# Performance work log

Measured on AMD Instinct MI355X. Metric: run time of the kernel, lower is better.

Reference implementation:

```python
import jax, jax.numpy as jnp
import numpy as np

B, S, H = 4, 2048, 512
DEPTH, EXP = 2, 4
MAX_LR = 0.1
C = 8            # n_chunks
L = S // C       # chunk length
HE = H * EXP


def _l2norm(x, eps=1e-12):
    n = jnp.sqrt(jnp.sum(x * x, axis=-1, keepdims=True))
    return x / jnp.maximum(n, eps)


def _mem_fwd(mw1, mb1, mw2, mb2, x):
    # ResLinear: residual MLP blocks, x <- x + W2 @ silu(W1 @ x + b1) + b2
    for d in range(DEPTH):
        h = jax.nn.silu(x @ mw1[d].T + mb1[d])
        x = x + h @ mw2[d].T + mb2[d]
    return x


def setup_inputs() -> dict:
    key = jax.random.key(0)
    ks = jax.random.split(key, 9)
    s = 1.0 / np.sqrt(H)
    s2 = 1.0 / np.sqrt(HE)
    return {
        "x": jax.random.normal(ks[0], (B, S, H), jnp.float32),
        "wq": jax.random.normal(ks[1], (H, H), jnp.float32) * s, "bq": jnp.zeros((H,), jnp.float32),
        "wk": jax.random.normal(ks[2], (H, H), jnp.float32) * s, "bk": jnp.zeros((H,), jnp.float32),
        "wv": jax.random.normal(ks[3], (H, H), jnp.float32) * s, "bv": jnp.zeros((H,), jnp.float32),
        "wlr": jax.random.normal(ks[4], (1, H), jnp.float32) * s, "blr": jnp.zeros((1,), jnp.float32),
        "wf": jax.random.normal(ks[5], (1, H), jnp.float32) * s, "bf": jnp.zeros((1,), jnp.float32),
        "wm": jax.random.normal(ks[6], (1, H), jnp.float32) * s, "bm": jnp.zeros((1,), jnp.float32),
        "mw1": jax.random.normal(ks[7], (DEPTH, HE, H), jnp.float32) * s,
        "mb1": jnp.zeros((DEPTH, HE), jnp.float32),
        "mw2": jax.random.normal(ks[8], (DEPTH, H, HE), jnp.float32) * s2,
        "mb2": jnp.zeros((DEPTH, H), jnp.float32),
        "mom_w1": jnp.zeros((DEPTH, HE, H), jnp.float32),
        "mom_b1": jnp.zeros((DEPTH, HE), jnp.float32),
        "mom_w2": jnp.zeros((DEPTH, H, HE), jnp.float32),
        "mom_b2": jnp.zeros((DEPTH, H), jnp.float32),
    }


def reference(x, wq, bq, wk, bk, wv, bv, wlr, blr, wf, bf, wm, bm,
              mw1, mb1, mw2, mb2, mom_w1, mom_b1, mom_w2, mom_b2):
    # projections (non-generating path; S % C == 0 so no padding)
    q = _l2norm(x @ wq.T + bq)                            # [B,S,H]
    k = _l2norm(x @ wk.T + bk).reshape(B, C, L, H)
    v = (x @ wv.T + bv).reshape(B, C, L, H)
    lr = jax.nn.sigmoid(x @ wlr.T + blr).reshape(B, C, L, 1) * MAX_LR
    forget = jax.nn.sigmoid(x @ wf.T + bf).reshape(B, C, L, 1)
    momg = jax.nn.sigmoid(x @ wm.T + bm).reshape(B, C, L, 1)

    mem = (mw1, mb1, mw2, mb2)

    def chunk_loss(mem_params, k_c, v_c, lr_c):
        # k_c,v_c: [B,L,H]; lr_c: [B,L,1]
        preds = _mem_fwd(*mem_params, k_c)
        loss = jnp.mean((preds - v_c) ** 2, axis=-1)      # [B,L]
        return jnp.sum(loss * lr_c[..., 0])

    # per-chunk synthetic gradients of the memory MLP, then mean over chunks
    grads = jax.vmap(jax.grad(chunk_loss), in_axes=(None, 1, 1, 1))(mem, k, v, lr)
    grads = jax.tree_util.tree_map(lambda g: jnp.mean(g, axis=0), grads)

    alpha = jnp.mean(forget, axis=(1, 2, 3))              # [B] forget gate
    theta = jnp.mean(lr, axis=(1, 2, 3))                  # [B] adaptive lr
    eta = jnp.mean(momg, axis=(1, 2, 3))                  # [B] momentum gate

    def update(p, g, m):
        shp = (B,) + (1,) * p.ndim
        a, t, e = alpha.reshape(shp), theta.reshape(shp), eta.reshape(shp)
        m_b = e * m[None] - t * g[None]                   # [B,*p.shape]
        return jnp.mean(p[None] * (1.0 - a) + m_b, axis=0)

    moms = (mom_w1, mom_b1, mom_w2, mom_b2)
    new_mem = tuple(update(p, g, m) for p, g, m in zip(mem, grads, moms))

    return _mem_fwd(*new_mem, q)                          # [B,S,H]
```

## Files before the change

### kernel.cpp

```cpp
#include <hip/hip_runtime.h>
#include <cstdint>
#include <cstddef>


#define NROWS 8192
#define HDIM  512
#define HEDIM 2048
#define NCHUNK 8
#define BK    64
#define DPCOEF (2.0f / (HDIM * NCHUNK))

typedef unsigned short u16;
typedef __attribute__((ext_vector_type(8))) unsigned short u16x8;
typedef __attribute__((ext_vector_type(8))) short bf16x8;
typedef __attribute__((ext_vector_type(4))) float f32x4;

__device__ __forceinline__ float sigmoidf_(float x){ return 1.0f/(1.0f+__expf(-x)); }
__device__ __forceinline__ float siluf_(float x){ return x*sigmoidf_(x); }
__device__ __forceinline__ float dsiluf_(float x){ float s=sigmoidf_(x); return s*(1.0f+x*(1.0f-s)); }
__device__ __forceinline__ u16 bf1_(float x){
    union{float f; unsigned u;} v; v.f = x;
    return (u16)((v.u + 0x7fffu + ((v.u>>16)&1u)) >> 16);
}
__device__ __forceinline__ unsigned bfpack_(float a, float b){
    union{float f; unsigned u;} ua, ub; ua.f = a; ub.f = b;
    unsigned ra = (ua.u + 0x7fffu + ((ua.u>>16)&1u)) >> 16;
    unsigned rb = (ub.u + 0x7fffu + ((ub.u>>16)&1u)) & 0xffff0000u;
    return ra | rb;
}
__device__ __forceinline__ float bf2f_(u16 h){
    union{unsigned u; float f;} v; v.u = ((unsigned)h) << 16; return v.f;
}
__device__ __forceinline__ int swkey_(int row){
    return (((row>>3)&1)<<2) | (((row>>4)&1)<<1) | ((row>>5)&1);
}
__device__ __forceinline__ void gl_lds16(const u16* g, u16* l){
    __builtin_amdgcn_global_load_lds(
        (const __attribute__((address_space(1))) unsigned*)g,
        (__attribute__((address_space(3))) unsigned*)l, 16, 0, 0);
}
__device__ __forceinline__ void bar_(){ asm volatile("s_barrier" ::: "memory"); }
#define VMCNT8  asm volatile("s_waitcnt vmcnt(8)" ::: "memory")
#define VMCNT0  asm volatile("s_waitcnt vmcnt(0)" ::: "memory")
#define LGKM0   asm volatile("s_waitcnt lgkmcnt(0)" ::: "memory")

template<int MODE, bool ATR, bool CSUM>
__global__ __launch_bounds__(256)
void mgemm_k(const u16* __restrict__ A, const u16* __restrict__ B,
             const float* __restrict__ bias, const float* __restrict__ resF,
             const u16* __restrict__ resB, const u16* __restrict__ aux,
             const float* __restrict__ lrs,
             float* __restrict__ outF, u16* __restrict__ outB, u16* __restrict__ outB2,
             float* __restrict__ cpart,
             int M, int N, int K, int lda, int ldb, int ldv)
{
    constexpr int NBUF = ATR ? 1 : 2;
    __shared__ __align__(128) u16 As[NBUF][128*64];
    __shared__ __align__(128) u16 Bs[NBUF][128*64];
    const int tid = threadIdx.x;
    const int lane = tid & 63, wvi = tid >> 6;
    const int wm = wvi >> 1, wn = wvi & 1;
    const int lr = lane & 15, lq = lane >> 4;

    const int gx = gridDim.x;
    const int nwg = gx * gridDim.y;
    int bid = blockIdx.y * gx + blockIdx.x;
    bid = (bid & 7) * (nwg >> 3) + (bid >> 3);
    const int m0 = (bid / gx) * 128, n0 = (bid % gx) * 128;

    int kbeg = 0, kend = K;
    if (MODE == 3){ const int ks = K >> 4; kbeg = blockIdx.z * ks; kend = kbeg + ks; }
    const int nk = (kend - kbeg) / BK;

    f32x4 acc[4][4];
    const f32x4 zz = {0.f,0.f,0.f,0.f};
    #pragma unroll
    for (int i = 0; i < 4; ++i)
        #pragma unroll
        for (int j = 0; j < 4; ++j) acc[i][j] = zz;

    const int mc = tid & 15, kp = tid >> 4;
    const int tkey = (((mc&1)<<2)|(((mc>>1)&1)<<1)|((mc>>2)&1));
    const int tcs = ((kp >> 1) ^ tkey) * 8 + (kp & 1) * 4;
    u16x8 rgA0, rgA1, rgA2, rgA3, rgB0, rgB1, rgB2, rgB3;

    auto stageNT = [&](int k0, int b){
        #pragma unroll
        for (int it = 0; it < 4; ++it){
            const int seg = it*4 + wvi;
            const int key = (((seg&1)<<2)|(((seg>>1)&1)<<1)|((seg>>2)&1));
            const int row = seg*8 + (lane>>3);
            const int chunk = (lane&7) ^ key;
            gl_lds16(A + (size_t)(m0+row)*lda + k0 + chunk*8, &As[b][seg*512]);
            gl_lds16(B + (size_t)(n0+row)*ldb + k0 + chunk*8, &Bs[b][seg*512]);
        }
    };
    auto gloadTN = [&](int k0){
        const u16* pa = A + (size_t)(k0 + 4*kp) * lda + m0 + mc*8;
        rgA0 = *(const u16x8*)pa;          rgA1 = *(const u16x8*)(pa + lda);
        rgA2 = *(const u16x8*)(pa+2*lda);  rgA3 = *(const u16x8*)(pa + 3*lda);
        const u16* pb = B + (size_t)(k0 + 4*kp) * ldb + n0 + mc*8;
        rgB0 = *(const u16x8*)pb;          rgB1 = *(const u16x8*)(pb + ldb);
        rgB2 = *(const u16x8*)(pb+2*ldb);  rgB3 = *(const u16x8*)(pb + 3*ldb);
    };
    auto dswriteTN = [&](){
        #pragma unroll
        for (int j = 0; j < 8; ++j){
            uint2 w;
            w.x = (unsigned)rgA0[j] | ((unsigned)rgA1[j] << 16);
            w.y = (unsigned)rgA2[j] | ((unsigned)rgA3[j] << 16);
            *(uint2*)&As[0][(mc*8 + j)*64 + tcs] = w;
            uint2 v;
            v.x = (unsigned)rgB0[j] | ((unsigned)rgB1[j] << 16);
            v.y = (unsigned)rgB2[j] | ((unsigned)rgB3[j] << 16);
            *(uint2*)&Bs[0][(mc*8 + j)*64 + tcs] = v;
        }
    };
    auto mfmaStep = [&](int b){
        #pragma unroll
        for (int ks = 0; ks < 2; ++ks) {
            bf16x8 afr[4], bfr[4];
            #pragma unroll
            for (int i = 0; i < 4; ++i){
                const int ra = wm*64 + i*16 + lr, rb = wn*64 + i*16 + lr;
                afr[i] = *(const bf16x8*)&As[b][ra*64 + (((ks*4 + lq) ^ swkey_(ra)) << 3)];
                bfr[i] = *(const bf16x8*)&Bs[b][rb*64 + (((ks*4 + lq) ^ swkey_(rb)) << 3)];
            }
            #pragma unroll
            for (int mi = 0; mi < 4; ++mi)
                #pragma unroll
                for (int ni = 0; ni < 4; ++ni)
                    acc[mi][ni] = __builtin_amdgcn_mfma_f32_16x16x32_bf16(afr[mi], bfr[ni], acc[mi][ni], 0, 0, 0);
        }
    };

    if (!ATR) {
        stageNT(kbeg, 0);
        int cur = 0;
        for (int i = 0; i < nk; ++i){
            const int k0 = kbeg + i*BK;
            if (i + 1 < nk){ stageNT(k0 + BK, cur ^ 1); VMCNT8; }
            else           { VMCNT0; }
            bar_();
            mfmaStep(cur);
            bar_();
            cur ^= 1;
        }
    } else {
        gloadTN(kbeg);
        dswriteTN();
        LGKM0;
        __syncthreads();
        for (int i = 0; i < nk; ++i){
            const int k0 = kbeg + i*BK;
            const bool hn = (i + 1 < nk);
            if (hn) gloadTN(k0 + BK);
            mfmaStep(0);
            __syncthreads();
            if (hn){ dswriteTN(); LGKM0; }
            __syncthreads();
        }
    }

    if (MODE == 3){
        unsigned* P32 = (unsigned*)outB;
        const size_t zb = (size_t)blockIdx.z * ((size_t)M * N / 2);
        #pragma unroll
        for (int ni = 0; ni < 4; ++ni){
            const int col = n0 + wn*64 + ni*16 + lr;
            #pragma unroll
            for (int mi = 0; mi < 4; ++mi){
                const int pr = (m0 + wm*64 + mi*16 + lq*4) >> 1;
                P32[zb + (size_t)pr*N + col]     = bfpack_(acc[mi][ni][0], acc[mi][ni][1]);
                P32[zb + (size_t)(pr+1)*N + col] = bfpack_(acc[mi][ni][2], acc[mi][ni][3]);
            }
        }
        return;
    }

    if (MODE == 7){
        #pragma unroll
        for (int ni = 0; ni < 4; ++ni){
            const int col = n0 + wn*64 + ni*16 + lr;
            const float bv = bias[col];
            #pragma unroll
            for (int mi = 0; mi < 4; ++mi){
                const int rbase = m0 + wm*64 + mi*16 + lq*4;
                #pragma unroll
                for (int v = 0; v < 4; ++v){
                    const size_t idx = (size_t)(rbase + v) * N + col;
                    outF[idx] = acc[mi][ni][v] + bv + resF[idx];
                }
            }
        }
        return;
    }

    u16*  S   = (u16*)&As[0][0];
    u16*  S2  = (u16*)&Bs[0][0];
    float* red = (float*)&Bs[0][0];
    float cs[4] = {0.f, 0.f, 0.f, 0.f};
    __syncthreads();
    #pragma unroll
    for (int ni = 0; ni < 4; ++ni){
        const int cl = wn*64 + ni*16 + lr;
        const int col = n0 + cl;
        float bv = 0.0f;
        if (MODE==1 || MODE==2 || MODE==6 || MODE==8 || MODE==9 || MODE==10) bv = bias[col];
        #pragma unroll
        for (int mi = 0; mi < 4; ++mi){
            #pragma unroll
            for (int v = 0; v < 4; ++v){
                const int rl = wm*64 + mi*16 + lq*4 + v;
                const int row = m0 + rl;
                const size_t idx = (size_t)row * N + col;
                const float o = acc[mi][ni][v];
                const int sidx = rl*128 + (cl ^ (((rl>>2)&3)<<4));
                float t;
                if (MODE == 1){
                    const float u = o + bv;
                    t = siluf_(u);
                    S2[sidx] = bf1_(dsiluf_(u));
                }
                else if (MODE == 2){ t = siluf_(o + bv); }
                else if (MODE == 4){ t = o * bf2f_(aux[idx]); if (CSUM) cs[ni] += t; }
                else if (MODE == 5){ t = o + bf2f_(resB[idx]); if (CSUM) cs[ni] += t; }
                else if (MODE == 6){ t = o + bv + resF[idx]; outF[idx] = t; }
                else if (MODE == 8){
                    const float u = o + bv + bf2f_(resB[idx]);
                    t = lrs[row] * DPCOEF * (u - bf2f_(aux[(size_t)row * ldv + col]));
                    if (CSUM) cs[ni] += t;
                }
                else if (MODE == 9){ t = o + bv + bf2f_(resB[idx]); }
                else { t = o + bv; }
                S[sidx] = bf1_(t);
            }
        }
    }
    if (CSUM){
        #pragma unroll
        for (int ni = 0; ni < 4; ++ni)
            red[(wm*4 + lq)*128 + wn*64 + ni*16 + lr] = cs[ni];
    }
    __syncthreads();
    #pragma unroll
    for (int j = 0; j < 8; ++j){
        const int ix = j*256 + tid;
        const int rl = ix >> 4, cc = (ix & 15) << 3;
        *(u16x8*)(outB + (size_t)(m0 + rl) * N + n0 + cc)
            = *(const u16x8*)&S[rl*128 + (cc ^ (((rl>>2)&3)<<4))];
    }
    if (MODE == 1){
        #pragma unroll
        for (int j = 0; j < 8; ++j){
            const int ix = j*256 + tid;
            const int rl = ix >> 4, cc = (ix & 15) << 3;
            *(u16x8*)(outB2 + (size_t)(m0 + rl) * N + n0 + cc)
                = *(const u16x8*)&S2[rl*128 + (cc ^ (((rl>>2)&3)<<4))];
        }
    }
    if (CSUM && tid < 128){
        float s = 0.f;
        #pragma unroll
        for (int z = 0; z < 8; ++z) s += red[z*128 + tid];
        cpart[(size_t)(m0 >> 7) * N + n0 + tid] = s;
    }
}

#define XSLOTS   (NROWS*HDIM/8)
#define W1S      (2*HEDIM*HDIM/8)
#define KVQSLOTS (3*HDIM*HDIM/8)
#define NB_EW    ((XSLOTS + 2*W1S + KVQSLOTS)/256 + 7)
#define TTILE    1024
__global__ __launch_bounds__(256)
void prep_all_k(const float* __restrict__ x,  u16* __restrict__ xb,
                const float* __restrict__ mw1, u16* __restrict__ mw1b,
                const float* __restrict__ mw2, u16* __restrict__ mw2b,
                const float* __restrict__ wk, const float* __restrict__ wv,
                const float* __restrict__ wq, u16* __restrict__ wkvqb,
                const float* __restrict__ bk, const float* __restrict__ bv,
                const float* __restrict__ bq, float* __restrict__ bkvq,
                u16* __restrict__ mw2Tb, u16* __restrict__ mw1T1b)
{
    __shared__ float tile[32][33];
    const int blk = blockIdx.x;
    if (blk >= NB_EW){
        int tj = blk - NB_EW;
        const float* in; u16* outp; int R, C;
        if (tj < TTILE){
            in = mw2; outp = mw2Tb; R = HDIM; C = HEDIM;
        } else if (tj < 2*TTILE){
            in = mw2 + (size_t)HDIM*HEDIM; outp = mw2Tb + (size_t)HEDIM*HDIM;
            R = HDIM; C = HEDIM; tj -= TTILE;
        } else {
            in = mw1 + (size_t)HEDIM*HDIM; outp = mw1T1b;
            R = HEDIM; C = HDIM; tj -= 2*TTILE;
        }
        const int tpc = C/32;
        const int r0 = (tj / tpc) * 32, c0 = (tj % tpc) * 32;
        const int tx = threadIdx.x & 31, ty = threadIdx.x >> 5;
        #pragma unroll
        for (int j = 0; j < 4; ++j)
            tile[ty + 8*j][tx] = in[(size_t)(r0 + ty + 8*j) * C + c0 + tx];
        __syncthreads();
        #pragma unroll
        for (int j = 0; j < 4; ++j)
            outp[(size_t)(c0 + ty + 8*j) * R + r0 + tx] = bf1_(tile[tx][ty + 8*j]);
        return;
    }
    const int id = blk * 256 + threadIdx.x;
    const float* src; u16* dst; int i;
    if (id < XSLOTS){ src = x; dst = xb; i = id; }
    else if (id < XSLOTS + W1S){ src = mw1; dst = mw1b; i = id - XSLOTS; }
    else if (id < XSLOTS + 2*W1S){ src = mw2; dst = mw2b; i = id - XSLOTS - W1S; }
    else if (id < XSLOTS + 2*W1S + KVQSLOTS){
        const int j = id - XSLOTS - 2*W1S;
        const int per = HDIM*HDIM/8;
        src = (j < per) ? wk : (j < 2*per ? wv : wq);
        i = (j < per) ? j : (j < 2*per ? j - per : j - 2*per);
        dst = wkvqb + ((size_t)(j - i)) * 8;
    }
    else {
        const int j = id - XSLOTS - 2*W1S - KVQSLOTS;
        if (j < 3*HDIM)
            bkvq[j] = (j < HDIM) ? bk[j] : (j < 2*HDIM ? bv[j-HDIM] : bq[j-2*HDIM]);
        return;
    }
    const float4 a = *(const float4*)(src + (size_t)i*8);
    const float4 b = *(const float4*)(src + (size_t)i*8 + 4);
    u16x8 o;
    o[0]=bf1_(a.x); o[1]=bf1_(a.y); o[2]=bf1_(a.z); o[3]=bf1_(a.w);
    o[4]=bf1_(b.x); o[5]=bf1_(b.y); o[6]=bf1_(b.z); o[7]=bf1_(b.w);
    *(u16x8*)(dst + (size_t)i*8) = o;
}

template<bool WF32>
__global__ __launch_bounds__(64)
void l2norm_k(const u16* __restrict__ in, int ld,
              float* __restrict__ outF, u16* __restrict__ outB)
{
    const u16* p = in + (size_t)blockIdx.x * ld;
    const int t = threadIdx.x;
    u16x8 v = *(const u16x8*)(p + t*8);
    float f[8];
    #pragma unroll
    for (int j = 0; j < 8; ++j) f[j] = bf2f_(v[j]);
    float s = 0.f;
    #pragma unroll
    for (int j = 0; j < 8; ++j) s += f[j]*f[j];
    #pragma unroll
    for (int o = 1; o < 64; o <<= 1) s += __shfl_xor(s, o);
    const float sc = 1.0f / fmaxf(sqrtf(s), 1e-12f);
    #pragma unroll
    for (int j = 0; j < 8; ++j) f[j] *= sc;
    if (WF32){
        float* q = outF + (size_t)blockIdx.x * HDIM + t*8;
        *(float4*)q     = make_float4(f[0], f[1], f[2], f[3]);
        *(float4*)(q+4) = make_float4(f[4], f[5], f[6], f[7]);
    }
    u16x8 ob;
    #pragma unroll
    for (int j = 0; j < 8; ++j) ob[j] = bf1_(f[j]);
    *(u16x8*)(outB + (size_t)blockIdx.x * HDIM + t*8) = ob;
}

__global__ __launch_bounds__(64)
void gates_k(const float* __restrict__ x,
             const float* __restrict__ wlr, const float* __restrict__ blr,
             const float* __restrict__ wf,  const float* __restrict__ bfp,
             const float* __restrict__ wm,  const float* __restrict__ bm,
             float* __restrict__ lr_s, float* __restrict__ f_s, float* __restrict__ m_s)
{
    const size_t row = blockIdx.x;
    const float* p = x + row * HDIM;
    const int t = threadIdx.x;
    float s0 = 0.f, s1 = 0.f, s2 = 0.f;
    #pragma unroll
    for (int i = 0; i < 8; i += 4){
        float4 xv = *(const float4*)(p   + t*8 + i);
        float4 a  = *(const float4*)(wlr + t*8 + i);
        float4 b  = *(const float4*)(wf  + t*8 + i);
        float4 c  = *(const float4*)(wm  + t*8 + i);
        s0 += xv.x*a.x + xv.y*a.y + xv.z*a.z + xv.w*a.w;
        s1 += xv.x*b.x + xv.y*b.y + xv.z*b.z + xv.w*b.w;
        s2 += xv.x*c.x + xv.y*c.y + xv.z*c.z + xv.w*c.w;
    }
    #pragma unroll
    for (int o = 1; o < 64; o <<= 1){
        s0 += __shfl_xor(s0, o); s1 += __shfl_xor(s1, o); s2 += __shfl_xor(s2, o);
    }
    if (t == 0){
        lr_s[row] = sigmoidf_(s0 + blr[0]) * 0.1f;
        f_s[row]  = sigmoidf_(s1 + bfp[0]);
        m_s[row]  = sigmoidf_(s2 + bm[0]);
    }
}

__global__ __launch_bounds__(256)
void scalars_k(const float* __restrict__ lr_s, const float* __restrict__ f_s,
               const float* __restrict__ m_s, float* __restrict__ sc)
{
    __shared__ float sh0[256], sh1[256], sh2[256];
    const int t = threadIdx.x;
    float s0 = 0.f, s1 = 0.f, s2 = 0.f;
    for (int i = t; i < NROWS; i += 256){ s0 += f_s[i]; s1 += lr_s[i]; s2 += m_s[i]; }
    sh0[t] = s0; sh1[t] = s1; sh2[t] = s2;
    __syncthreads();
    for (int o = 128; o > 0; o >>= 1){
        if (t < o){ sh0[t] += sh0[t+o]; sh1[t] += sh1[t+o]; sh2[t] += sh2[t+o]; }
        __syncthreads();
    }
    if (t == 0){
        sc[0] = sh0[0] / (float)NROWS;
        sc[1] = sh1[0] / (float)NROWS;
        sc[2] = sh2[0] / (float)NROWS;
    }
}

__global__ __launch_bounds__(256)
void colsum_upd_k(const float* __restrict__ part, const float* __restrict__ p,
                  const float* __restrict__ mom, const float* __restrict__ sc,
                  float* __restrict__ nb, int cols)
{
    const int c = blockIdx.x * 256 + threadIdx.x;
    if (c < cols){
        float s = 0.f;
        for (int r = 0; r < 64; ++r) s += part[(size_t)r * cols + c];
        nb[c] = p[c] * (1.0f - sc[0]) + sc[2] * mom[c] - sc[1] * s;
    }
}

__global__ __launch_bounds__(256)
void fupdate16p_k(const float* __restrict__ p, const unsigned* __restrict__ P32,
                  const float* __restrict__ mom, const float* __restrict__ sc,
                  u16* __restrict__ nWb, int N, int MN2)
{
    const int i = blockIdx.x * 256 + threadIdx.x;
    if (i < MN2){
        float g0 = 0.f, g1 = 0.f;
        #pragma unroll
        for (int z = 0; z < 16; ++z){
            const unsigned w = P32[(size_t)z * MN2 + i];
            g0 += bf2f_((u16)(w & 0xffffu));
            g1 += bf2f_((u16)(w >> 16));
        }
        const int c = i & (N - 1);
        const size_t r0 = ((size_t)(i / N) * 2) * N + c;
        nWb[r0]     = bf1_(p[r0]     * (1.0f - sc[0]) + sc[2] * mom[r0]     - sc[1] * g0);
        nWb[r0 + N] = bf1_(p[r0 + N] * (1.0f - sc[0]) + sc[2] * mom[r0 + N] - sc[1] * g1);
    }
}

extern "C" void kernel_launch(void* const* d_in, const int* in_sizes, int n_in,
                              void* d_out, int out_size, void* d_ws, size_t ws_size,
                              hipStream_t stream)
{
    const float* x      = (const float*)d_in[0];
    const float* wq     = (const float*)d_in[1];
    const float* bq     = (const float*)d_in[2];
    const float* wk     = (const float*)d_in[3];
    const float* bk     = (const float*)d_in[4];
    const float* wv     = (const float*)d_in[5];
    const float* bv     = (const float*)d_in[6];
    const float* wlr    = (const float*)d_in[7];
    const float* blr    = (const float*)d_in[8];
    const float* wf     = (const float*)d_in[9];
    const float* bfp    = (const float*)d_in[10];
    const float* wm     = (const float*)d_in[11];
    const float* bm     = (const float*)d_in[12];
    const float* mw1    = (const float*)d_in[13];
    const float* mb1    = (const float*)d_in[14];
    const float* mw2    = (const float*)d_in[15];
    const float* mb2    = (const float*)d_in[16];
    const float* mom_w1 = (const float*)d_in[17];
    const float* mom_b1 = (const float*)d_in[18];
    const float* mom_w2 = (const float*)d_in[19];
    const float* mom_b2 = (const float*)d_in[20];
    float* out = (float*)d_out;

    char* base = (char*)d_ws;
    size_t off = 0;
    auto alloc = [&](size_t bytes)->char*{ char* p = base + off; off += (bytes + 255) & ~(size_t)255; return p; };
    const size_t NHf  = (size_t)NROWS * HDIM  * 4;
    const size_t NHb  = (size_t)NROWS * HDIM  * 2;
    const size_t NHEb = (size_t)NROWS * HEDIM * 2;
    const int    WHALF = HEDIM * HDIM;

    float* F2   = (float*)alloc(NHf);
    u16*  xb    = (u16*) alloc(NHb);
    u16*  kb    = (u16*) alloc(NHb);
    u16*  x1b   = (u16*) alloc(NHb);
    u16*  g2b   = (u16*) alloc(NHb);
    u16*  hb    = (u16*) alloc(NHEb);
    u16*  db    = (u16*) alloc(NHEb);
    u16*  dhb   = (u16*) alloc(NHEb + NHf);
    u16*  wkvqb = (u16*) alloc((size_t)3*HDIM*HDIM*2);
    float* bkvq = (float*)alloc((size_t)3*HDIM*4);
    u16*  mw1b  = (u16*) alloc((size_t)2*WHALF*2);
    u16*  mw2b  = (u16*) alloc((size_t)2*WHALF*2);
    u16*  mw2Tb = (u16*) alloc((size_t)2*WHALF*2);
    u16*  mw1T1b= (u16*) alloc((size_t)WHALF*2);
    u16*  nW1b  = (u16*) alloc((size_t)2*WHALF*2);
    u16*  nW2b  = (u16*) alloc((size_t)2*WHALF*2);
    float* cpart= (float*)alloc((size_t)64*HEDIM*4);
    float* lr_s = (float*)alloc((size_t)NROWS*4);
    float* f_s  = (float*)alloc((size_t)NROWS*4);
    float* m_s  = (float*)alloc((size_t)NROWS*4);
    float* sc   = (float*)alloc(64);
    float* nb1  = (float*)alloc((size_t)2*HEDIM*4);
    float* nb2  = (float*)alloc((size_t)2*HDIM*4);

    u16* qb  = xb;
    u16* g1b = g2b;
    u16* P3b = dhb;
    float* F1 = (float*)((char*)dhb + NHEb);
    unsigned* Pp = (unsigned*)db;

    const dim3 blk(256);
    const dim3 gKVQ (3*HDIM/128, NROWS/128);
    const dim3 gN512 (HDIM/128,  NROWS/128);
    const dim3 gN2048(HEDIM/128, NROWS/128);
    const dim3 gTN2  (HEDIM/128, HDIM/128, 16);
    const dim3 gTN1  (HDIM/128,  HEDIM/128, 16);
    const int MN2 = WHALF / 2;

    const float* mw1_1 = mw1 + (size_t)WHALF;
    const float* mw2_1 = mw2 + (size_t)WHALF;

    #define GARG(Ab,Bb,bi,rF,rB,ax,ll,oF,oB,oB2,cp,M,N,K,la,lb,lv) \
        ((const u16*)(Ab),(const u16*)(Bb),(const float*)(bi),(const float*)(rF),\
         (const u16*)(rB),(const u16*)(ax),(const float*)(ll),\
         (float*)(oF),(u16*)(oB),(u16*)(oB2),(float*)(cp),(M),(N),(K),(la),(lb),(lv))

    prep_all_k<<<dim3(NB_EW + 3*TTILE), blk, 0, stream>>>(
        x, xb, mw1, mw1b, mw2, mw2b, wk, wv, wq, wkvqb,
        bk, bv, bq, bkvq, mw2Tb, mw1T1b);
    gates_k<<<NROWS, 64, 0, stream>>>(x, wlr, blr, wf, bfp, wm, bm, lr_s, f_s, m_s);
    scalars_k<<<1, blk, 0, stream>>>(lr_s, f_s, m_s, sc);

    mgemm_k<10,false,false><<<gKVQ, blk, 0, stream>>>GARG(xb, wkvqb, bkvq, 0,0,0,0, 0, P3b, 0, 0, NROWS,3*HDIM,HDIM, HDIM,HDIM, 0);
    l2norm_k<false><<<NROWS, 64, 0, stream>>>(P3b,          3*HDIM, nullptr, kb);
    l2norm_k<true ><<<NROWS, 64, 0, stream>>>(P3b + 2*HDIM, 3*HDIM, F2, qb);

    mgemm_k<2,false,false><<<gN2048, blk, 0, stream>>>GARG(kb, mw1b, mb1, 0,0,0,0, 0, hb, 0, 0, NROWS,HEDIM,HDIM, HDIM,HDIM, 0);
    mgemm_k<9,false,false><<<gN512, blk, 0, stream>>>GARG(hb, mw2b, mb2, 0, kb, 0,0, 0, x1b, 0, 0, NROWS,HDIM,HEDIM, HEDIM,HEDIM, 0);
    mgemm_k<1,false,false><<<gN2048, blk, 0, stream>>>GARG(x1b, mw1b+WHALF, mb1+HEDIM, 0,0,0,0, 0, hb, db, 0, NROWS,HEDIM,HDIM, HDIM,HDIM, 0);
    mgemm_k<8,false,true><<<gN512, blk, 0, stream>>>GARG(hb, mw2b+WHALF, mb2+HDIM, 0, x1b, P3b + HDIM, lr_s, 0, g2b, 0, cpart, NROWS,HDIM,HEDIM, HEDIM,HEDIM, 3*HDIM);

    colsum_upd_k<<<dim3(HDIM/256), blk, 0, stream>>>(cpart, mb2+HDIM, mom_b2+HDIM, sc, nb2+HDIM, HDIM);
    mgemm_k<4,false,true><<<gN2048, blk, 0, stream>>>GARG(g2b, mw2Tb+WHALF, 0,0,0, db, 0, 0, dhb, 0, cpart, NROWS,HEDIM,HDIM, HDIM,HDIM, 0);
    mgemm_k<3,true,false><<<gTN2, blk, 0, stream>>>GARG(g2b, hb, 0,0,0,0,0, 0, Pp, 0, 0, HDIM,HEDIM,NROWS, HDIM,HEDIM, 0);
    fupdate16p_k<<<dim3((MN2+255)/256), blk, 0, stream>>>(mw2_1, Pp, mom_w2+WHALF, sc, nW2b+WHALF, HEDIM, MN2);
    colsum_upd_k<<<dim3(HEDIM/256), blk, 0, stream>>>(cpart, mb1+HEDIM, mom_b1+HEDIM, sc, nb1+HEDIM, HEDIM);
    mgemm_k<3,true,false><<<gTN1, blk, 0, stream>>>GARG(dhb, x1b, 0,0,0,0,0, 0, Pp, 0, 0, HEDIM,HDIM,NROWS, HEDIM,HDIM, 0);
    fupdate16p_k<<<dim3((MN2+255)/256), blk, 0, stream>>>(mw1_1, Pp, mom_w1+WHALF, sc, nW1b+WHALF, HDIM, MN2);
    mgemm_k<5,false,true><<<gN512, blk, 0, stream>>>GARG(dhb, mw1T1b, 0, 0, g2b, 0, 0, 0, g1b, 0, cpart, NROWS,HDIM,HEDIM, HEDIM,HEDIM, 0);

    colsum_upd_k<<<dim3(HDIM/256), blk, 0, stream>>>(cpart, mb2, mom_b2, sc, nb2, HDIM);
    mgemm_k<1,false,false><<<gN2048, blk, 0, stream>>>GARG(kb, mw1b, mb1, 0,0,0,0, 0, hb, db, 0, NROWS,HEDIM,HDIM, HDIM,HDIM, 0);
    mgemm_k<4,false,true><<<gN2048, blk, 0, stream>>>GARG(g1b, mw2Tb, 0,0,0, db, 0, 0, dhb, 0, cpart, NROWS,HEDIM,HDIM, HDIM,HDIM, 0);
    mgemm_k<3,true,false><<<gTN2, blk, 0, stream>>>GARG(g1b, hb, 0,0,0,0,0, 0, Pp, 0, 0, HDIM,HEDIM,NROWS, HDIM,HEDIM, 0);
    fupdate16p_k<<<dim3((MN2+255)/256), blk, 0, stream>>>(mw2, Pp, mom_w2, sc, nW2b, HEDIM, MN2);
    colsum_upd_k<<<dim3(HEDIM/256), blk, 0, stream>>>(cpart, mb1, mom_b1, sc, nb1, HEDIM);
    mgemm_k<3,true,false><<<gTN1, blk, 0, stream>>>GARG(dhb, kb, 0,0,0,0,0, 0, Pp, 0, 0, HEDIM,HDIM,NROWS, HEDIM,HDIM, 0);
    fupdate16p_k<<<dim3((MN2+255)/256), blk, 0, stream>>>(mw1, Pp, mom_w1, sc, nW1b, HDIM, MN2);

    mgemm_k<2,false,false><<<gN2048, blk, 0, stream>>>GARG(qb, nW1b, nb1, 0,0,0,0, 0, hb, 0, 0, NROWS,HEDIM,HDIM, HDIM,HDIM, 0);
    mgemm_k<6,false,false><<<gN512, blk, 0, stream>>>GARG(hb, nW2b, nb2, F2, 0,0,0, F1, x1b, 0, 0, NROWS,HDIM,HEDIM, HEDIM,HEDIM, 0);
    mgemm_k<2,false,false><<<gN2048, blk, 0, stream>>>GARG(x1b, nW1b+WHALF, nb1+HEDIM, 0,0,0,0, 0, hb, 0, 0, NROWS,HEDIM,HDIM, HDIM,HDIM, 0);
    mgemm_k<7,false,false><<<gN512, blk, 0, stream>>>GARG(hb, nW2b+WHALF, nb2+HDIM, F1, 0,0,0, out, 0, 0, 0, NROWS,HDIM,HEDIM, HEDIM,HEDIM, 0);

    #undef GARG
    (void)in_sizes; (void)n_in; (void)out_size; (void)ws_size;
}
```

Before: 687.7 us.

## Use 64x128 two-wave tiles for the N=512 GEMMs to fill more CUs

Adds a WAVES template parameter to the GEMM kernel. For the long-K GEMMs with N=512, the M tile shrinks from 128 to 64 rows and the block drops from four waves to two, which doubles the number of workgroups. The staging loops, vmcnt waits, epilogue indexing and column-sum partial counts are adjusted to match, and colsum_upd_k now takes the partial count as a parameter. The aim is to give the skinny-N GEMMs enough workgroups to occupy all CUs, at the cost of less B-tile reuse per block and more column-sum partials to reduce.

```diff
diff --git a/kernel.cpp b/kernel.cpp
--- a/kernel.cpp
+++ b/kernel.cpp
@@ -40,12 +40,13 @@
         (__attribute__((address_space(3))) unsigned*)l, 16, 0, 0);
 }
 __device__ __forceinline__ void bar_(){ asm volatile("s_barrier" ::: "memory"); }
+#define VMCNT12 asm volatile("s_waitcnt vmcnt(12)" ::: "memory")
 #define VMCNT8  asm volatile("s_waitcnt vmcnt(8)" ::: "memory")
 #define VMCNT0  asm volatile("s_waitcnt vmcnt(0)" ::: "memory")
 #define LGKM0   asm volatile("s_waitcnt lgkmcnt(0)" ::: "memory")
 
-template<int MODE, bool ATR, bool CSUM>
-__global__ __launch_bounds__(256)
+template<int MODE, bool ATR, bool CSUM, int WAVES>
+__global__ __launch_bounds__(WAVES*64)
 void mgemm_k(const u16* __restrict__ A, const u16* __restrict__ B,
              const float* __restrict__ bias, const float* __restrict__ resF,
              const u16* __restrict__ resB, const u16* __restrict__ aux,
@@ -55,18 +56,22 @@
              int M, int N, int K, int lda, int ldb, int ldv)
 {
     constexpr int NBUF = ATR ? 1 : 2;
-    __shared__ __align__(128) u16 As[NBUF][128*64];
+    constexpr int MT   = (WAVES == 4) ? 128 : 64;
+    constexpr int NT_  = WAVES * 64;
+    __shared__ __align__(128) u16 As[NBUF][MT*64];
     __shared__ __align__(128) u16 Bs[NBUF][128*64];
     const int tid = threadIdx.x;
     const int lane = tid & 63, wvi = tid >> 6;
-    const int wm = wvi >> 1, wn = wvi & 1;
+    const int wm = (WAVES == 4) ? (wvi >> 1) : 0;
+    const int wn = (WAVES == 4) ? (wvi & 1) : wvi;
+    constexpr int WNW = (WAVES == 4) ? 2 : 2;
     const int lr = lane & 15, lq = lane >> 4;
 
     const int gx = gridDim.x;
     const int nwg = gx * gridDim.y;
     int bid = blockIdx.y * gx + blockIdx.x;
     bid = (bid & 7) * (nwg >> 3) + (bid >> 3);
-    const int m0 = (bid / gx) * 128, n0 = (bid % gx) * 128;
+    const int m0 = (bid / gx) * MT, n0 = (bid % gx) * 128;
 
     int kbeg = 0, kend = K;
     if (MODE == 3){ const int ks = K >> 4; kbeg = blockIdx.z * ks; kend = kbeg + ks; }
@@ -86,12 +91,19 @@
 
     auto stageNT = [&](int k0, int b){
         #pragma unroll
-        for (int it = 0; it < 4; ++it){
-            const int seg = it*4 + wvi;
+        for (int it = 0; it < (MT/8)/WAVES; ++it){
+            const int seg = it*WAVES + wvi;
             const int key = (((seg&1)<<2)|(((seg>>1)&1)<<1)|((seg>>2)&1));
             const int row = seg*8 + (lane>>3);
             const int chunk = (lane&7) ^ key;
             gl_lds16(A + (size_t)(m0+row)*lda + k0 + chunk*8, &As[b][seg*512]);
+        }
+        #pragma unroll
+        for (int it = 0; it < 16/WAVES; ++it){
+            const int seg = it*WAVES + wvi;
+            const int key = (((seg&1)<<2)|(((seg>>1)&1)<<1)|((seg>>2)&1));
+            const int row = seg*8 + (lane>>3);
+            const int chunk = (lane&7) ^ key;
             gl_lds16(B + (size_t)(n0+row)*ldb + k0 + chunk*8, &Bs[b][seg*512]);
         }
     };
@@ -139,8 +151,10 @@
         int cur = 0;
         for (int i = 0; i < nk; ++i){
             const int k0 = kbeg + i*BK;
-            if (i + 1 < nk){ stageNT(k0 + BK, cur ^ 1); VMCNT8; }
-            else           { VMCNT0; }
+            if (i + 1 < nk){
+                stageNT(k0 + BK, cur ^ 1);
+                if (WAVES == 4) { VMCNT8; } else { VMCNT12; }
+            } else { VMCNT0; }
             bar_();
             mfmaStep(cur);
             bar_();
@@ -199,6 +213,7 @@
     u16*  S   = (u16*)&As[0][0];
     u16*  S2  = (u16*)&Bs[0][0];
     float* red = (float*)&Bs[0][0];
+    constexpr int RED = (WAVES == 4) ? 8 : 4;
     float cs[4] = {0.f, 0.f, 0.f, 0.f};
     __syncthreads();
     #pragma unroll
@@ -245,7 +260,7 @@
     __syncthreads();
     #pragma unroll
     for (int j = 0; j < 8; ++j){
-        const int ix = j*256 + tid;
+        const int ix = j*NT_ + tid;
         const int rl = ix >> 4, cc = (ix & 15) << 3;
         *(u16x8*)(outB + (size_t)(m0 + rl) * N + n0 + cc)
             = *(const u16x8*)&S[rl*128 + (cc ^ (((rl>>2)&3)<<4))];
@@ -253,7 +268,7 @@
     if (MODE == 1){
         #pragma unroll
         for (int j = 0; j < 8; ++j){
-            const int ix = j*256 + tid;
+            const int ix = j*NT_ + tid;
             const int rl = ix >> 4, cc = (ix & 15) << 3;
             *(u16x8*)(outB2 + (size_t)(m0 + rl) * N + n0 + cc)
                 = *(const u16x8*)&S2[rl*128 + (cc ^ (((rl>>2)&3)<<4))];
@@ -262,8 +277,8 @@
     if (CSUM && tid < 128){
         float s = 0.f;
         #pragma unroll
-        for (int z = 0; z < 8; ++z) s += red[z*128 + tid];
-        cpart[(size_t)(m0 >> 7) * N + n0 + tid] = s;
+        for (int z = 0; z < RED; ++z) s += red[z*128 + tid];
+        cpart[(size_t)(m0 / MT) * N + n0 + tid] = s;
     }
 }
 
@@ -420,12 +435,12 @@
 __global__ __launch_bounds__(256)
 void colsum_upd_k(const float* __restrict__ part, const float* __restrict__ p,
                   const float* __restrict__ mom, const float* __restrict__ sc,
-                  float* __restrict__ nb, int cols)
+                  float* __restrict__ nb, int cols, int nparts)
 {
     const int c = blockIdx.x * 256 + threadIdx.x;
     if (c < cols){
         float s = 0.f;
-        for (int r = 0; r < 64; ++r) s += part[(size_t)r * cols + c];
+        for (int r = 0; r < nparts; ++r) s += part[(size_t)r * cols + c];
         nb[c] = p[c] * (1.0f - sc[0]) + sc[2] * mom[c] - sc[1] * s;
     }
 }
@@ -516,10 +531,10 @@
     float* F1 = (float*)((char*)dhb + NHEb);
     unsigned* Pp = (unsigned*)db;
 
-    const dim3 blk(256);
-    const dim3 gKVQ (3*HDIM/128, NROWS/128);
-    const dim3 gN512 (HDIM/128,  NROWS/128);
-    const dim3 gN2048(HEDIM/128, NROWS/128);
+    const dim3 blk(256), blk2(128);
+    const dim3 gKVQ  (3*HDIM/128, NROWS/128);
+    const dim3 gN512 (HDIM/128,   NROWS/64);
+    const dim3 gN2048(HEDIM/128,  NROWS/128);
     const dim3 gTN2  (HEDIM/128, HDIM/128, 16);
     const dim3 gTN1  (HDIM/128,  HEDIM/128, 16);
     const int MN2 = WHALF / 2;
@@ -538,37 +553,37 @@
     gates_k<<<NROWS, 64, 0, stream>>>(x, wlr, blr, wf, bfp, wm, bm, lr_s, f_s, m_s);
     scalars_k<<<1, blk, 0, stream>>>(lr_s, f_s, m_s, sc);
 
-    mgemm_k<10,false,false><<<gKVQ, blk, 0, stream>>>GARG(xb, wkvqb, bkvq, 0,0,0,0, 0, P3b, 0, 0, NROWS,3*HDIM,HDIM, HDIM,HDIM, 0);
+    mgemm_k<10,false,false,4><<<gKVQ, blk, 0, stream>>>GARG(xb, wkvqb, bkvq, 0,0,0,0, 0, P3b, 0, 0, NROWS,3*HDIM,HDIM, HDIM,HDIM, 0);
     l2norm_k<false><<<NROWS, 64, 0, stream>>>(P3b,          3*HDIM, nullptr, kb);
     l2norm_k<true ><<<NROWS, 64, 0, stream>>>(P3b + 2*HDIM, 3*HDIM, F2, qb);
 
-    mgemm_k<2,false,false><<<gN2048, blk, 0, stream>>>GARG(kb, mw1b, mb1, 0,0,0,0, 0, hb, 0, 0, NROWS,HEDIM,HDIM, HDIM,HDIM, 0);
-    mgemm_k<9,false,false><<<gN512, blk, 0, stream>>>GARG(hb, mw2b, mb2, 0, kb, 0,0, 0, x1b, 0, 0, NROWS,HDIM,HEDIM, HEDIM,HEDIM, 0);
-    mgemm_k<1,false,false><<<gN2048, blk, 0, stream>>>GARG(x1b, mw1b+WHALF, mb1+HEDIM, 0,0,0,0, 0, hb, db, 0, NROWS,HEDIM,HDIM, HDIM,HDIM, 0);
-    mgemm_k<8,false,true><<<gN512, blk, 0, stream>>>GARG(hb, mw2b+WHALF, mb2+HDIM, 0, x1b, P3b + HDIM, lr_s, 0, g2b, 0, cpart, NROWS,HDIM,HEDIM, HEDIM,HEDIM, 3*HDIM);
-
-    colsum_upd_k<<<dim3(HDIM/256), blk, 0, stream>>>(cpart, mb2+HDIM, mom_b2+HDIM, sc, nb2+HDIM, HDIM);
-    mgemm_k<4,false,true><<<gN2048, blk, 0, stream>>>GARG(g2b, mw2Tb+WHALF, 0,0,0, db, 0, 0, dhb, 0, cpart, NROWS,HEDIM,HDIM, HDIM,HDIM, 0);
-    mgemm_k<3,true,false><<<gTN2, blk, 0, stream>>>GARG(g2b, hb, 0,0,0,0,0, 0, Pp, 0, 0, HDIM,HEDIM,NROWS, HDIM,HEDIM, 0);
+    mgemm_k<2,false,false,4><<<gN2048, blk, 0, stream>>>GARG(kb, mw1b, mb1, 0,0,0,0, 0, hb, 0, 0, NROWS,HEDIM,HDIM, HDIM,HDIM, 0);
+    mgemm_k<9,false,false,2><<<gN512, blk2, 0, stream>>>GARG(hb, mw2b, mb2, 0, kb, 0,0, 0, x1b, 0, 0, NROWS,HDIM,HEDIM, HEDIM,HEDIM, 0);
+    mgemm_k<1,false,false,4><<<gN2048, blk, 0, stream>>>GARG(x1b, mw1b+WHALF, mb1+HEDIM, 0,0,0,0, 0, hb, db, 0, NROWS,HEDIM,HDIM, HDIM,HDIM, 0);
+    mgemm_k<8,false,true,2><<<gN512, blk2, 0, stream>>>GARG(hb, mw2b+WHALF, mb2+HDIM, 0, x1b, P3b + HDIM, lr_s, 0, g2b, 0, cpart, NROWS,HDIM,HEDIM, HEDIM,HEDIM, 3*HDIM);
+
+    colsum_upd_k<<<dim3(HDIM/256), blk, 0, stream>>>(cpart, mb2+HDIM, mom_b2+HDIM, sc, nb2+HDIM, HDIM, 128);
+    mgemm_k<4,false,true,4><<<gN2048, blk, 0, stream>>>GARG(g2b, mw2Tb+WHALF, 0,0,0, db, 0, 0, dhb, 0, cpart, NROWS,HEDIM,HDIM, HDIM,HDIM, 0);
+    mgemm_k<3,true,false,4><<<gTN2, blk, 0, stream>>>GARG(g2b, hb, 0,0,0,0,0, 0, Pp, 0, 0, HDIM,HEDIM,NROWS, HDIM,HEDIM, 0);
     fupdate16p_k<<<dim3((MN2+255)/256), blk, 0, stream>>>(mw2_1, Pp, mom_w2+WHALF, sc, nW2b+WHALF, HEDIM, MN2);
-    colsum_upd_k<<<dim3(HEDIM/256), blk, 0, stream>>>(cpart, mb1+HEDIM, mom_b1+HEDIM, sc, nb1+HEDIM, HEDIM);
-    mgemm_k<3,true,false><<<gTN1, blk, 0, stream>>>GARG(dhb, x1b, 0,0,0,0,0, 0, Pp, 0, 0, HEDIM,HDIM,NROWS, HEDIM,HDIM, 0);
+    colsum_upd_k<<<dim3(HEDIM/256), blk, 0, stream>>>(cpart, mb1+HEDIM, mom_b1+HEDIM, sc, nb1+HEDIM, HEDIM, 64);
+    mgemm_k<3,true,false,4><<<gTN1, blk, 0, stream>>>GARG(dhb, x1b, 0,0,0,0,0, 0, Pp, 0, 0, HEDIM,HDIM,NROWS, HEDIM,HDIM, 0);
     fupdate16p_k<<<dim3((MN2+255)/256), blk, 0, stream>>>(mw1_1, Pp, mom_w1+WHALF, sc, nW1b+WHALF, HDIM, MN2);
-    mgemm_k<5,false,true><<<gN512, blk, 0, stream>>>GARG(dhb, mw1T1b, 0, 0, g2b, 0, 0, 0, g1b, 0, cpart, NROWS,HDIM,HEDIM, HEDIM,HEDIM, 0);
-
-    colsum_upd_k<<<dim3(HDIM/256), blk, 0, stream>>>(cpart, mb2, mom_b2, sc, nb2, HDIM);
-    mgemm_k<1,false,false><<<gN2048, blk, 0, stream>>>GARG(kb, mw1b, mb1, 0,0,0,0, 0, hb, db, 0, NROWS,HEDIM,HDIM, HDIM,HDIM, 0);
-    mgemm_k<4,false,true><<<gN2048, blk, 0, stream>>>GARG(g1b, mw2Tb, 0,0,0, db, 0, 0, dhb, 0, cpart, NROWS,HEDIM,HDIM, HDIM,HDIM, 0);
-    mgemm_k<3,true,false><<<gTN2, blk, 0, stream>>>GARG(g1b, hb, 0,0,0,0,0, 0, Pp, 0, 0, HDIM,HEDIM,NROWS, HDIM,HEDIM, 0);
+    mgemm_k<5,false,true,2><<<gN512, blk2, 0, stream>>>GARG(dhb, mw1T1b, 0, 0, g2b, 0, 0, 0, g1b, 0, cpart, NROWS,HDIM,HEDIM, HEDIM,HEDIM, 0);
+
+    colsum_upd_k<<<dim3(HDIM/256), blk, 0, stream>>>(cpart, mb2, mom_b2, sc, nb2, HDIM, 128);
+    mgemm_k<1,false,false,4><<<gN2048, blk, 0, stream>>>GARG(kb, mw1b, mb1, 0,0,0,0, 0, hb, db, 0, NROWS,HEDIM,HDIM, HDIM,HDIM, 0);
+    mgemm_k<4,false,true,4><<<gN2048, blk, 0, stream>>>GARG(g1b, mw2Tb, 0,0,0, db, 0, 0, dhb, 0, cpart, NROWS,HEDIM,HDIM, HDIM,HDIM, 0);
+    mgemm_k<3,true,false,4><<<gTN2, blk, 0, stream>>>GARG(g1b, hb, 0,0,0,0,0, 0, Pp, 0, 0, HDIM,HEDIM,NROWS, HDIM,HEDIM, 0);
     fupdate16p_k<<<dim3((MN2+255)/256), blk, 0, stream>>>(mw2, Pp, mom_w2, sc, nW2b, HEDIM, MN2);
-    colsum_upd_k<<<dim3(HEDIM/256), blk, 0, stream>>>(cpart, mb1, mom_b1, sc, nb1, HEDIM);
-    mgemm_k<3,true,false><<<gTN1, blk, 0, stream>>>GARG(dhb, kb, 0,0,0,0,0, 0, Pp, 0, 0, HEDIM,HDIM,NROWS, HEDIM,HDIM, 0);
+    colsum_upd_k<<<dim3(HEDIM/256), blk, 0, stream>>>(cpart, mb1, mom_b1, sc, nb1, HEDIM, 64);
+    mgemm_k<3,true,false,4><<<gTN1, blk, 0, stream>>>GARG(dhb, kb, 0,0,0,0,0, 0, Pp, 0, 0, HEDIM,HDIM,NROWS, HEDIM,HDIM, 0);
     fupdate16p_k<<<dim3((MN2+255)/256), blk, 0, stream>>>(mw1, Pp, mom_w1, sc, nW1b, HDIM, MN2);
 
-    mgemm_k<2,false,false><<<gN2048, blk, 0, stream>>>GARG(qb, nW1b, nb1, 0,0,0,0, 0, hb, 0, 0, NROWS,HEDIM,HDIM, HDIM,HDIM, 0);
-    mgemm_k<6,false,false><<<gN512, blk, 0, stream>>>GARG(hb, nW2b, nb2, F2, 0,0,0, F1, x1b, 0, 0, NROWS,HDIM,HEDIM, HEDIM,HEDIM, 0);
-    mgemm_k<2,false,false><<<gN2048, blk, 0, stream>>>GARG(x1b, nW1b+WHALF, nb1+HEDIM, 0,0,0,0, 0, hb, 0, 0, NROWS,HEDIM,HDIM, HDIM,HDIM, 0);
-    mgemm_k<7,false,false><<<gN512, blk, 0, stream>>>GARG(hb, nW2b+WHALF, nb2+HDIM, F1, 0,0,0, out, 0, 0, 0, NROWS,HDIM,HEDIM, HEDIM,HEDIM, 0);
+    mgemm_k<2,false,false,4><<<gN2048, blk, 0, stream>>>GARG(qb, nW1b, nb1, 0,0,0,0, 0, hb, 0, 0, NROWS,HEDIM,HDIM, HDIM,HDIM, 0);
+    mgemm_k<6,false,false,2><<<gN512, blk2, 0, stream>>>GARG(hb, nW2b, nb2, F2, 0,0,0, F1, x1b, 0, 0, NROWS,HDIM,HEDIM, HEDIM,HEDIM, 0);
+    mgemm_k<2,false,false,4><<<gN2048, blk, 0, stream>>>GARG(x1b, nW1b+WHALF, nb1+HEDIM, 0,0,0,0, 0, hb, 0, 0, NROWS,HEDIM,HDIM, HDIM,HDIM, 0);
+    mgemm_k<7,false,false,2><<<gN512, blk2, 0, stream>>>GARG(hb, nW2b+WHALF, nb2+HDIM, F1, 0,0,0, out, 0, 0, 0, NROWS,HDIM,HEDIM, HEDIM,HEDIM, 0);
 
     #undef GARG
     (void)in_sizes; (void)n_in; (void)out_size; (void)ws_size;
```

After: 765.4 us. 1.11x slower.
